# Kernel optimization log

Hardware: AMD Instinct MI355X
Metric: run time of the kernel (lower is better)

## Reference

```python
import jax, jax.numpy as jnp
import numpy as np

S, B, H = 50, 2048, 128
D = 2 * H  # bidirectional hidden width


def _xavier(k, shape):
    fan = float(sum(shape))
    return jax.random.normal(k, shape, dtype=jnp.float32) * jnp.float32(np.sqrt(2.0 / fan))


def setup_inputs() -> dict:
    key = jax.random.key(0)
    ks = jax.random.split(key, 16)
    z = lambda n: jnp.zeros((n,), jnp.float32)
    return {
        "encoder_output": jax.random.normal(ks[0], (S, B, D), jnp.float32),
        "h0": jax.random.normal(ks[1], (2, B, H), jnp.float32),
        "c0": jax.random.normal(ks[2], (2, B, H), jnp.float32),
        "restricted_k": jax.random.uniform(ks[3], (B,), jnp.float32, 0.5, 1.5),
        "W_first": _xavier(ks[4], (D, 2)), "b_first": z(D),
        "Wih_f": _xavier(ks[5], (4 * H, D)), "Whh_f": _xavier(ks[6], (4 * H, H)),
        "bih_f": z(4 * H), "bhh_f": z(4 * H),
        "Wih_b": _xavier(ks[7], (4 * H, D)), "Whh_b": _xavier(ks[8], (4 * H, H)),
        "bih_b": z(4 * H), "bhh_b": z(4 * H),
        "Wref_g": _xavier(ks[9], (D, D)), "Wq_g": _xavier(ks[10], (D, D)),
        "vg": jax.random.uniform(ks[11], (D,), jnp.float32),
        "Wref": _xavier(ks[12], (D, D)), "Wq": _xavier(ks[13], (D, D)),
        "v": jax.random.uniform(ks[14], (D,), jnp.float32),
    }


def _lstm_cell(x, h, c, Wih, Whh, bih, bhh):
    # PyTorch gate order: i, f, g, o
    g = x @ Wih.T + h @ Whh.T + bih + bhh
    i, f, gg, o = jnp.split(g, 4, axis=-1)
    c2 = jax.nn.sigmoid(f) * c + jax.nn.sigmoid(i) * jnp.tanh(gg)
    h2 = jax.nn.sigmoid(o) * jnp.tanh(c2)
    return h2, c2


def reference(encoder_output, h0, c0, restricted_k, W_first, b_first,
              Wih_f, Whh_f, bih_f, bhh_f, Wih_b, Whh_b, bih_b, bhh_b,
              Wref_g, Wq_g, vg, Wref, Wq, v):
    S_, B_, D_ = encoder_output.shape
    total_iter = S_ - 1  # mode == 'k'

    # first_entry: [1.1, 1/restricted_k] -> Linear(2, 2H) -> tanh, detached
    fe = jnp.stack([jnp.full((B_,), 1.1, jnp.float32), 1.0 / restricted_k], axis=1)
    dec_ipt0 = jax.lax.stop_gradient(jnp.tanh(fe @ W_first.T + b_first))  # [B, D]

    # ref-side attention projections are constant across decode steps
    ref_g_dot = jnp.einsum('de,sbe->bds', Wref_g, encoder_output)  # [B, D, S]
    ref_p_dot = jnp.einsum('de,sbe->bds', Wref, encoder_output)    # [B, D, S]

    mask0 = jnp.zeros((B_, S_), jnp.float32)
    NEG = -jnp.inf

    def step(carry, _):
        dec_ipt, h, c, mask = carry
        hf, cf = _lstm_cell(dec_ipt, h[0], c[0], Wih_f, Whh_f, bih_f, bhh_f)
        hb, cb = _lstm_cell(dec_ipt, h[1], c[1], Wih_b, Whh_b, bih_b, bhh_b)
        q = jnp.concatenate([hf, hb], axis=-1)  # [B, D] (len-1 bi-LSTM output)
        h2 = jnp.stack([hf, hb]); c2 = jnp.stack([cf, cb])
        maskb = mask > 0
        # glimpse attention
        u_g = jnp.einsum('d,bds->bs', vg, jnp.tanh(ref_g_dot + (q @ Wq_g.T)[:, :, None]))
        a = jax.nn.softmax(jnp.where(maskb, NEG, u_g), axis=1)  # [B, S]
        g_l = jnp.einsum('sbd,bs->bd', encoder_output, a)
        # pointer attention
        u_p = jnp.einsum('d,bds->bs', v, jnp.tanh(ref_p_dot + (g_l @ Wq.T)[:, :, None]))
        logits = jnp.where(maskb, NEG, u_p)
        sel = jnp.argmax(logits, axis=1)  # config.selection == 'argmax'
        lp = jnp.take_along_axis(jax.nn.log_softmax(logits, axis=1), sel[:, None], axis=1)[:, 0]
        mask2 = mask + jax.nn.one_hot(sel, S_, dtype=mask.dtype)
        new_ipt = encoder_output[sel, jnp.arange(B_)]  # [B, D]
        return (new_ipt, h2, c2, mask2), (sel, lp)

    _, (sels, lps) = jax.lax.scan(step, (dec_ipt0, h0, c0, mask0), None, length=total_iter)
    selections = jnp.transpose(sels)          # [B, total_iter]
    log_probs = jnp.sum(lps, axis=0)          # [B]
    return selections, log_probs
```

## Files before the change

kernel.cpp:

```cpp
#include <hip/hip_runtime.h>
#include <math.h>

#define SS 50
#define BB 2048
#define HH 128
#define DD 256
#define STEPS 49
#define NREF ((size_t)BB * SS * DD)

__device__ __forceinline__ float sigmoidf_(float x) { return 1.0f / (1.0f + expf(-x)); }

__global__ __launch_bounds__(256) void k_init(
    const float* __restrict__ h0, const float* __restrict__ c0,
    const float* __restrict__ rk, const float* __restrict__ Wf,
    const float* __restrict__ bf,
    float* __restrict__ x, float* __restrict__ q, float* __restrict__ c,
    int* __restrict__ unm, float* __restrict__ lp)
{
    int idx = blockIdx.x * 256 + threadIdx.x;
    int b = idx >> 8, d = idx & 255;
    float inv = 1.0f / rk[b];
    float t0 = 1.1f * Wf[2 * d] + inv * Wf[2 * d + 1];
    x[idx] = tanhf(t0 + bf[d]);
    q[idx] = (d < HH) ? h0[b * HH + d] : h0[BB * HH + b * HH + (d - HH)];
    c[idx] = c0[idx];
    if (idx < BB * 64) unm[idx] = idx & 63;
    if (idx < BB) lp[idx] = 0.0f;
}

__global__ __launch_bounds__(256) void k_refdot(
    const float* __restrict__ enc, const float* __restrict__ Wg,
    const float* __restrict__ Wp, const float* __restrict__ Wqq,
    float* __restrict__ refg, float* __restrict__ refp, float* __restrict__ refq)
{
    const float* W = (blockIdx.z == 0) ? Wg : (blockIdx.z == 1) ? Wp : Wqq;
    float* out = (blockIdx.z == 0) ? refg : (blockIdx.z == 1) ? refp : refq;
    __shared__ float As[16][68];
    __shared__ float Ws[16][264];
    int t = threadIdx.x;
    int m0 = blockIdx.x * 64;
    int rr = t >> 2, kk = (t & 3) << 2;
    int n = m0 + rr;
    int ab = n / SS, as = n - ab * SS;
    const float* arow = enc + ((size_t)as * BB + ab) * DD + kk;
    const float* wrow = W + (size_t)t * DD;
    int tm = (t & 15) << 2;
    int tn = (t >> 4) << 4;
    float acc[4][16];
#pragma unroll
    for (int i = 0; i < 4; i++)
#pragma unroll
        for (int j = 0; j < 16; j++) acc[i][j] = 0.0f;

    for (int k0 = 0; k0 < DD; k0 += 16) {
        float4 av = *(const float4*)(arow + k0);
        float4 w0 = *(const float4*)(wrow + k0);
        float4 w1 = *(const float4*)(wrow + k0 + 4);
        float4 w2 = *(const float4*)(wrow + k0 + 8);
        float4 w3 = *(const float4*)(wrow + k0 + 12);
        __syncthreads();
        As[kk + 0][rr] = av.x; As[kk + 1][rr] = av.y;
        As[kk + 2][rr] = av.z; As[kk + 3][rr] = av.w;
        Ws[0][t] = w0.x;  Ws[1][t] = w0.y;  Ws[2][t] = w0.z;  Ws[3][t] = w0.w;
        Ws[4][t] = w1.x;  Ws[5][t] = w1.y;  Ws[6][t] = w1.z;  Ws[7][t] = w1.w;
        Ws[8][t] = w2.x;  Ws[9][t] = w2.y;  Ws[10][t] = w2.z; Ws[11][t] = w2.w;
        Ws[12][t] = w3.x; Ws[13][t] = w3.y; Ws[14][t] = w3.z; Ws[15][t] = w3.w;
        __syncthreads();
#pragma unroll
        for (int k = 0; k < 16; k++) {
            float4 a = *(const float4*)&As[k][tm];
            float aa[4] = {a.x, a.y, a.z, a.w};
#pragma unroll
            for (int jj = 0; jj < 4; jj++) {
                float4 w = *(const float4*)&Ws[k][tn + (jj << 2)];
                float ww[4] = {w.x, w.y, w.z, w.w};
#pragma unroll
                for (int i = 0; i < 4; i++)
#pragma unroll
                    for (int cj = 0; cj < 4; cj++)
                        acc[i][jj * 4 + cj] = fmaf(aa[i], ww[cj], acc[i][jj * 4 + cj]);
            }
        }
    }
#pragma unroll
    for (int i = 0; i < 4; i++) {
        float* orow = out + (size_t)(m0 + tm + i) * DD + tn;
#pragma unroll
        for (int jj = 0; jj < 4; jj++) {
            float4 o = make_float4(acc[i][jj * 4], acc[i][jj * 4 + 1],
                                   acc[i][jj * 4 + 2], acc[i][jj * 4 + 3]);
            *(float4*)(orow + (jj << 2)) = o;
        }
    }
}

__global__ __launch_bounds__(256) void k_gates(
    const float* __restrict__ x, const float* __restrict__ q,
    const float* __restrict__ Wih_f, const float* __restrict__ Whh_f,
    const float* __restrict__ bih_f, const float* __restrict__ bhh_f,
    const float* __restrict__ Wih_b, const float* __restrict__ Whh_b,
    const float* __restrict__ bih_b, const float* __restrict__ bhh_b,
    float* __restrict__ gates)
{
    int z = blockIdx.z;
    const float* Wih = z ? Wih_b : Wih_f;
    const float* Whh = z ? Whh_b : Whh_f;
    const float* bih = z ? bih_b : bih_f;
    const float* bhh = z ? bhh_b : bhh_f;
    __shared__ float As[16][68];
    __shared__ float Ws[16][68];
    int t = threadIdx.x;
    int m0 = blockIdx.x * 64, n0 = blockIdx.y * 64;
    int rr = t >> 2, kk = (t & 3) << 2;
    int tm = (t & 15) << 2, tn = (t >> 4) << 2;
    float acc[4][4] = {};
    for (int k0 = 0; k0 < 384; k0 += 16) {
        float4 av, wv;
        if (k0 < 256) {
            av = *(const float4*)(x + (size_t)(m0 + rr) * DD + k0 + kk);
            wv = *(const float4*)(Wih + (size_t)(n0 + rr) * DD + k0 + kk);
        } else {
            av = *(const float4*)(q + (size_t)(m0 + rr) * DD + (z << 7) + (k0 - 256) + kk);
            wv = *(const float4*)(Whh + (size_t)(n0 + rr) * HH + (k0 - 256) + kk);
        }
        __syncthreads();
        As[kk + 0][rr] = av.x; As[kk + 1][rr] = av.y;
        As[kk + 2][rr] = av.z; As[kk + 3][rr] = av.w;
        Ws[kk + 0][rr] = wv.x; Ws[kk + 1][rr] = wv.y;
        Ws[kk + 2][rr] = wv.z; Ws[kk + 3][rr] = wv.w;
        __syncthreads();
#pragma unroll
        for (int k = 0; k < 16; k++) {
            float4 a = *(const float4*)&As[k][tm];
            float4 w = *(const float4*)&Ws[k][tn];
            float aa[4] = {a.x, a.y, a.z, a.w};
            float ww[4] = {w.x, w.y, w.z, w.w};
#pragma unroll
            for (int i = 0; i < 4; i++)
#pragma unroll
                for (int j = 0; j < 4; j++)
                    acc[i][j] = fmaf(aa[i], ww[j], acc[i][j]);
        }
    }
#pragma unroll
    for (int i = 0; i < 4; i++) {
        int col = n0 + tn;
        float4 o;
        o.x = acc[i][0] + bih[col + 0] + bhh[col + 0];
        o.y = acc[i][1] + bih[col + 1] + bhh[col + 1];
        o.z = acc[i][2] + bih[col + 2] + bhh[col + 2];
        o.w = acc[i][3] + bih[col + 3] + bhh[col + 3];
        *(float4*)(gates + (size_t)(m0 + tm + i) * 1024 + (z << 9) + col) = o;
    }
}

__global__ __launch_bounds__(256) void k_lstm_pw(
    const float* __restrict__ gates, float* __restrict__ q, float* __restrict__ c)
{
    int idx = blockIdx.x * 256 + threadIdx.x;
    int z = idx >> 18;
    int r = idx & (BB * HH - 1);
    int b = r >> 7, hh = r & 127;
    const float* gb = gates + (size_t)b * 1024 + (z << 9);
    float ig = sigmoidf_(gb[hh]);
    float fg = sigmoidf_(gb[128 + hh]);
    float gg = tanhf(gb[256 + hh]);
    float og = sigmoidf_(gb[384 + hh]);
    float c2 = fg * c[idx] + ig * gg;
    c[idx] = c2;
    q[(size_t)b * DD + (z << 7) + hh] = og * tanhf(c2);
}

__global__ __launch_bounds__(256) void k_proj(
    const float* __restrict__ A, const float* __restrict__ W, float* __restrict__ out)
{
    __shared__ float As[16][68];
    __shared__ float Ws[16][68];
    int t = threadIdx.x;
    int m0 = blockIdx.x * 64, n0 = blockIdx.y * 64;
    int rr = t >> 2, kk = (t & 3) << 2;
    int tm = (t & 15) << 2, tn = (t >> 4) << 2;
    const float* arow = A + (size_t)(m0 + rr) * DD + kk;
    const float* wrow = W + (size_t)(n0 + rr) * DD + kk;
    float acc[4][4] = {};
    for (int k0 = 0; k0 < DD; k0 += 16) {
        float4 av = *(const float4*)(arow + k0);
        float4 wv = *(const float4*)(wrow + k0);
        __syncthreads();
        As[kk + 0][rr] = av.x; As[kk + 1][rr] = av.y;
        As[kk + 2][rr] = av.z; As[kk + 3][rr] = av.w;
        Ws[kk + 0][rr] = wv.x; Ws[kk + 1][rr] = wv.y;
        Ws[kk + 2][rr] = wv.z; Ws[kk + 3][rr] = wv.w;
        __syncthreads();
#pragma unroll
        for (int k = 0; k < 16; k++) {
            float4 a = *(const float4*)&As[k][tm];
            float4 w = *(const float4*)&Ws[k][tn];
            float aa[4] = {a.x, a.y, a.z, a.w};
            float ww[4] = {w.x, w.y, w.z, w.w};
#pragma unroll
            for (int i = 0; i < 4; i++)
#pragma unroll
                for (int j = 0; j < 4; j++)
                    acc[i][j] = fmaf(aa[i], ww[j], acc[i][j]);
        }
    }
#pragma unroll
    for (int i = 0; i < 4; i++) {
        float4 o = make_float4(acc[i][0], acc[i][1], acc[i][2], acc[i][3]);
        *(float4*)(out + (size_t)(m0 + tm + i) * DD + n0 + tn) = o;
    }
}

__global__ __launch_bounds__(256) void k_glimpse(
    const float* __restrict__ refg, const float* __restrict__ qW,
    const float* __restrict__ vg, const float* __restrict__ enc,
    const int* __restrict__ unm, float* __restrict__ a,
    float* __restrict__ gl, int cnt)
{
    int b = blockIdx.x;
    int t = threadIdx.x, wave = t >> 6, lane = t & 63;
    __shared__ float ash[SS];
    __shared__ int sl[SS];
    if (t < cnt) sl[t] = unm[b * 64 + t];
    __syncthreads();
    int d0 = lane << 2;
    float4 qw = *(const float4*)(qW + (size_t)b * DD + d0);
    float4 vv = *(const float4*)(vg + d0);
    for (int li = wave; li < cnt; li += 4) {
        int s = sl[li];
        float4 r = *(const float4*)(refg + ((size_t)b * SS + s) * DD + d0);
        float sum = vv.x * tanhf(r.x + qw.x) + vv.y * tanhf(r.y + qw.y) +
                    vv.z * tanhf(r.z + qw.z) + vv.w * tanhf(r.w + qw.w);
#pragma unroll
        for (int off = 32; off; off >>= 1) sum += __shfl_xor(sum, off);
        if (lane == 0) ash[li] = sum;
    }
    __syncthreads();
    if (t < 64) {
        float logit = (t < cnt) ? ash[t] : -__builtin_inff();
        float m = logit;
#pragma unroll
        for (int off = 32; off; off >>= 1) m = fmaxf(m, __shfl_xor(m, off));
        float e = expf(logit - m);
        float ssum = e;
#pragma unroll
        for (int off = 32; off; off >>= 1) ssum += __shfl_xor(ssum, off);
        if (t < cnt) {
            float av = e / ssum;
            ash[t] = av;
            a[b * 64 + t] = av;
        }
    }
    __syncthreads();
    if (gl) {
        float accv = 0.0f;
        for (int li = 0; li < cnt; ++li)
            accv = fmaf(ash[li], enc[((size_t)sl[li] * BB + b) * DD + t], accv);
        gl[(size_t)b * DD + t] = accv;
    }
}

__global__ __launch_bounds__(256) void k_pointer(
    const float* __restrict__ refp, const float* __restrict__ refq,
    const float* __restrict__ gWin, const float* __restrict__ vp,
    const float* __restrict__ enc, int* __restrict__ unm,
    const float* __restrict__ a, float* __restrict__ lp,
    float* __restrict__ x, float* __restrict__ outp, int step, int cnt)
{
    int b = blockIdx.x;
    int t = threadIdx.x, wave = t >> 6, lane = t & 63;
    __shared__ float ash[SS];
    __shared__ int sl[SS];
    __shared__ float gw[DD];
    __shared__ int ssel;
    if (t < cnt) { sl[t] = unm[b * 64 + t]; ash[t] = a[b * 64 + t]; }
    __syncthreads();
    if (refq) {
        float accg = 0.0f;
        for (int li = 0; li < cnt; ++li)
            accg = fmaf(ash[li], refq[((size_t)b * SS + sl[li]) * DD + t], accg);
        gw[t] = accg;
    } else {
        gw[t] = gWin[(size_t)b * DD + t];
    }
    __syncthreads();
    int d0 = lane << 2;
    float4 g4 = *(const float4*)(gw + d0);
    float4 vv = *(const float4*)(vp + d0);
    for (int li = wave; li < cnt; li += 4) {
        int s = sl[li];
        float4 r = *(const float4*)(refp + ((size_t)b * SS + s) * DD + d0);
        float sum = vv.x * tanhf(r.x + g4.x) + vv.y * tanhf(r.y + g4.y) +
                    vv.z * tanhf(r.z + g4.z) + vv.w * tanhf(r.w + g4.w);
#pragma unroll
        for (int off = 32; off; off >>= 1) sum += __shfl_xor(sum, off);
        if (lane == 0) ash[li] = sum;
    }
    __syncthreads();
    if (t < 64) {
        float logit = (t < cnt) ? ash[t] : -__builtin_inff();
        int skey = (t < cnt) ? (sl[t] * 64 + t) : (1 << 30);
        float m = logit;
#pragma unroll
        for (int off = 32; off; off >>= 1) m = fmaxf(m, __shfl_xor(m, off));
        int cand = (logit == m) ? skey : (1 << 30);
#pragma unroll
        for (int off = 32; off; off >>= 1) cand = min(cand, __shfl_xor(cand, off));
        float e = expf(logit - m);
        float se = e;
#pragma unroll
        for (int off = 32; off; off >>= 1) se += __shfl_xor(se, off);
        if (t == 0) {
            int s_sel = cand >> 6, posl = cand & 63;
            float lpn = lp[b] - logf(se);
            lp[b] = lpn;
            outp[(size_t)b * STEPS + step] = (float)s_sel;
            if (step == STEPS - 1) outp[(size_t)BB * STEPS + b] = lpn;
            unm[b * 64 + posl] = sl[cnt - 1];
            ssel = s_sel;
        }
    }
    __syncthreads();
    x[(size_t)b * DD + t] = enc[((size_t)ssel * BB + b) * DD + t];
}

extern "C" void kernel_launch(void* const* d_in, const int* in_sizes, int n_in,
                              void* d_out, int out_size, void* d_ws, size_t ws_size,
                              hipStream_t stream) {
    const float* enc    = (const float*)d_in[0];
    const float* h0     = (const float*)d_in[1];
    const float* c0     = (const float*)d_in[2];
    const float* rk     = (const float*)d_in[3];
    const float* Wfirst = (const float*)d_in[4];
    const float* bfirst = (const float*)d_in[5];
    const float* Wih_f  = (const float*)d_in[6];
    const float* Whh_f  = (const float*)d_in[7];
    const float* bih_f  = (const float*)d_in[8];
    const float* bhh_f  = (const float*)d_in[9];
    const float* Wih_b  = (const float*)d_in[10];
    const float* Whh_b  = (const float*)d_in[11];
    const float* bih_b  = (const float*)d_in[12];
    const float* bhh_b  = (const float*)d_in[13];
    const float* Wref_g = (const float*)d_in[14];
    const float* Wq_g   = (const float*)d_in[15];
    const float* vg     = (const float*)d_in[16];
    const float* Wref   = (const float*)d_in[17];
    const float* Wq     = (const float*)d_in[18];
    const float* v      = (const float*)d_in[19];
    float* out = (float*)d_out;

    float* ws    = (float*)d_ws;
    float* refg  = ws;
    float* refp  = refg + NREF;
    float* x     = refp + NREF;
    float* q     = x + (size_t)BB * DD;
    float* c     = q + (size_t)BB * DD;
    float* gates = c + (size_t)BB * DD;
    float* qWb   = gates + (size_t)BB * 1024;
    float* gl    = qWb + (size_t)BB * DD;
    float* gWb   = gl + (size_t)BB * DD;
    float* a     = gWb + (size_t)BB * DD;
    float* lp    = a + (size_t)BB * 64;
    int*   unm   = (int*)(lp + BB);
    float* refq  = (float*)(unm + (size_t)BB * 64);

    size_t need_refq = ((size_t)(refq - ws) + NREF) * sizeof(float);
    bool useRefq = ws_size >= need_refq;

    k_init<<<dim3(BB * DD / 256), dim3(256), 0, stream>>>(h0, c0, rk, Wfirst,
                                                          bfirst, x, q, c, unm, lp);
    k_refdot<<<dim3(BB * SS / 64, 1, useRefq ? 3 : 2), dim3(256), 0, stream>>>(
        enc, Wref_g, Wref, Wq, refg, refp, refq);
    for (int step = 0; step < STEPS; ++step) {
        int cnt = SS - step;
        k_gates<<<dim3(32, 8, 2), dim3(256), 0, stream>>>(
            x, q, Wih_f, Whh_f, bih_f, bhh_f, Wih_b, Whh_b, bih_b, bhh_b, gates);
        k_lstm_pw<<<dim3(2 * BB * HH / 256), dim3(256), 0, stream>>>(gates, q, c);
        k_proj<<<dim3(32, 4), dim3(256), 0, stream>>>(q, Wq_g, qWb);
        k_glimpse<<<dim3(BB), dim3(256), 0, stream>>>(refg, qWb, vg, enc, unm, a,
                                                      useRefq ? nullptr : gl, cnt);
        if (!useRefq)
            k_proj<<<dim3(32, 4), dim3(256), 0, stream>>>(gl, Wq, gWb);
        k_pointer<<<dim3(BB), dim3(256), 0, stream>>>(refp, useRefq ? refq : nullptr,
                                                      gWb, v, enc, unm, a, lp, x, out,
                                                      step, cnt);
    }
}
```

Measured before the change: 4.834 ms.

## Fuse LSTM gate GEMM with pointwise cell and merge attention kernels

The gate GEMM now computes all four gates for a tile of hidden units so the LSTM cell update runs in its epilogue, with q double-buffered so the pointwise kernel and the gates buffer go away. The query projection, glimpse attention, pointer projection and pointer attention are merged into one per-batch-row kernel that computes q·Wq_g with a per-row matrix-vector product instead of a separate tiled GEMM. This cuts six launches per step to two and drops several intermediate global round trips. In exchange, each of the 2048 blocks rereads the full 256x256 Wq_g from cache, and the gate GEMM grid shrinks to 256 blocks.

```diff
diff --git a/kernel.cpp b/kernel.cpp
--- a/kernel.cpp
+++ b/kernel.cpp
@@ -94,151 +94,147 @@
     }
 }
 
-__global__ __launch_bounds__(256) void k_gates(
-    const float* __restrict__ x, const float* __restrict__ q,
+__global__ __launch_bounds__(256) void k_gates2(
+    const float* __restrict__ x, const float* __restrict__ qin,
     const float* __restrict__ Wih_f, const float* __restrict__ Whh_f,
     const float* __restrict__ bih_f, const float* __restrict__ bhh_f,
     const float* __restrict__ Wih_b, const float* __restrict__ Whh_b,
     const float* __restrict__ bih_b, const float* __restrict__ bhh_b,
-    float* __restrict__ gates)
+    float* __restrict__ qout, float* __restrict__ c)
 {
     int z = blockIdx.z;
     const float* Wih = z ? Wih_b : Wih_f;
     const float* Whh = z ? Whh_b : Whh_f;
     const float* bih = z ? bih_b : bih_f;
     const float* bhh = z ? bhh_b : bhh_f;
-    __shared__ float As[16][68];
-    __shared__ float Ws[16][68];
+    int m0 = blockIdx.x * 32;
+    int hc0 = blockIdx.y * 64;
     int t = threadIdx.x;
-    int m0 = blockIdx.x * 64, n0 = blockIdx.y * 64;
-    int rr = t >> 2, kk = (t & 3) << 2;
-    int tm = (t & 15) << 2, tn = (t >> 4) << 2;
-    float acc[4][4] = {};
+    int mb4 = (t >> 5) << 2;
+    int hp2 = (t & 31) << 1;
+    __shared__ float As[16][33];
+    __shared__ float Ws[16][258];
+    float acc[4][4][2] = {};
+
     for (int k0 = 0; k0 < 384; k0 += 16) {
-        float4 av, wv;
+        float4 av;
+        int am = t >> 2, ak = (t & 3) << 2;
+        if (t < 128) {
+            if (k0 < 256)
+                av = *(const float4*)(x + (size_t)(m0 + am) * DD + k0 + ak);
+            else
+                av = *(const float4*)(qin + (size_t)(m0 + am) * DD + (z << 7) + (k0 - 256) + ak);
+        }
+        int g = t >> 6, hc = t & 63;
+        int r = g * 128 + hc0 + hc;
+        float4 w0, w1, w2, w3;
         if (k0 < 256) {
-            av = *(const float4*)(x + (size_t)(m0 + rr) * DD + k0 + kk);
-            wv = *(const float4*)(Wih + (size_t)(n0 + rr) * DD + k0 + kk);
+            const float* wr = Wih + (size_t)r * DD + k0;
+            w0 = *(const float4*)(wr);     w1 = *(const float4*)(wr + 4);
+            w2 = *(const float4*)(wr + 8); w3 = *(const float4*)(wr + 12);
         } else {
-            av = *(const float4*)(q + (size_t)(m0 + rr) * DD + (z << 7) + (k0 - 256) + kk);
-            wv = *(const float4*)(Whh + (size_t)(n0 + rr) * HH + (k0 - 256) + kk);
-        }
-        __syncthreads();
-        As[kk + 0][rr] = av.x; As[kk + 1][rr] = av.y;
-        As[kk + 2][rr] = av.z; As[kk + 3][rr] = av.w;
-        Ws[kk + 0][rr] = wv.x; Ws[kk + 1][rr] = wv.y;
-        Ws[kk + 2][rr] = wv.z; Ws[kk + 3][rr] = wv.w;
-        __syncthreads();
-#pragma unroll
-        for (int k = 0; k < 16; k++) {
-            float4 a = *(const float4*)&As[k][tm];
-            float4 w = *(const float4*)&Ws[k][tn];
-            float aa[4] = {a.x, a.y, a.z, a.w};
-            float ww[4] = {w.x, w.y, w.z, w.w};
-#pragma unroll
-            for (int i = 0; i < 4; i++)
-#pragma unroll
-                for (int j = 0; j < 4; j++)
-                    acc[i][j] = fmaf(aa[i], ww[j], acc[i][j]);
-        }
-    }
-#pragma unroll
-    for (int i = 0; i < 4; i++) {
-        int col = n0 + tn;
-        float4 o;
-        o.x = acc[i][0] + bih[col + 0] + bhh[col + 0];
-        o.y = acc[i][1] + bih[col + 1] + bhh[col + 1];
-        o.z = acc[i][2] + bih[col + 2] + bhh[col + 2];
-        o.w = acc[i][3] + bih[col + 3] + bhh[col + 3];
-        *(float4*)(gates + (size_t)(m0 + tm + i) * 1024 + (z << 9) + col) = o;
-    }
-}
-
-__global__ __launch_bounds__(256) void k_lstm_pw(
-    const float* __restrict__ gates, float* __restrict__ q, float* __restrict__ c)
+            const float* wr = Whh + (size_t)r * HH + (k0 - 256);
+            w0 = *(const float4*)(wr);     w1 = *(const float4*)(wr + 4);
+            w2 = *(const float4*)(wr + 8); w3 = *(const float4*)(wr + 12);
+        }
+        __syncthreads();
+        if (t < 128) {
+            As[ak + 0][am] = av.x; As[ak + 1][am] = av.y;
+            As[ak + 2][am] = av.z; As[ak + 3][am] = av.w;
+        }
+        Ws[0][t] = w0.x;  Ws[1][t] = w0.y;  Ws[2][t] = w0.z;  Ws[3][t] = w0.w;
+        Ws[4][t] = w1.x;  Ws[5][t] = w1.y;  Ws[6][t] = w1.z;  Ws[7][t] = w1.w;
+        Ws[8][t] = w2.x;  Ws[9][t] = w2.y;  Ws[10][t] = w2.z; Ws[11][t] = w2.w;
+        Ws[12][t] = w3.x; Ws[13][t] = w3.y; Ws[14][t] = w3.z; Ws[15][t] = w3.w;
+        __syncthreads();
+#pragma unroll
+        for (int k = 0; k < 16; ++k) {
+            float a0 = As[k][mb4 + 0];
+            float a1 = As[k][mb4 + 1];
+            float a2 = As[k][mb4 + 2];
+            float a3 = As[k][mb4 + 3];
+#pragma unroll
+            for (int g2 = 0; g2 < 4; ++g2) {
+                float2 wv = *(const float2*)&Ws[k][(g2 << 6) + hp2];
+                acc[0][g2][0] = fmaf(a0, wv.x, acc[0][g2][0]);
+                acc[0][g2][1] = fmaf(a0, wv.y, acc[0][g2][1]);
+                acc[1][g2][0] = fmaf(a1, wv.x, acc[1][g2][0]);
+                acc[1][g2][1] = fmaf(a1, wv.y, acc[1][g2][1]);
+                acc[2][g2][0] = fmaf(a2, wv.x, acc[2][g2][0]);
+                acc[2][g2][1] = fmaf(a2, wv.y, acc[2][g2][1]);
+                acc[3][g2][0] = fmaf(a3, wv.x, acc[3][g2][0]);
+                acc[3][g2][1] = fmaf(a3, wv.y, acc[3][g2][1]);
+            }
+        }
+    }
+#pragma unroll
+    for (int i = 0; i < 4; ++i) {
+#pragma unroll
+        for (int cc = 0; cc < 2; ++cc) {
+            int b = m0 + mb4 + i;
+            int h = hc0 + hp2 + cc;
+            float gi = acc[i][0][cc] + bih[h]       + bhh[h];
+            float gf = acc[i][1][cc] + bih[128 + h] + bhh[128 + h];
+            float gg = acc[i][2][cc] + bih[256 + h] + bhh[256 + h];
+            float go = acc[i][3][cc] + bih[384 + h] + bhh[384 + h];
+            size_t cidx = (size_t)z * BB * HH + (size_t)b * HH + h;
+            float c2 = sigmoidf_(gf) * c[cidx] + sigmoidf_(gi) * tanhf(gg);
+            c[cidx] = c2;
+            qout[(size_t)b * DD + (z << 7) + h] = sigmoidf_(go) * tanhf(c2);
+        }
+    }
+}
+
+__global__ __launch_bounds__(256) void k_attn(
+    const float* __restrict__ refg, const float* __restrict__ refp,
+    const float* __restrict__ refq, const float* __restrict__ q,
+    const float* __restrict__ Wqg, const float* __restrict__ vg,
+    const float* __restrict__ Wqp, const float* __restrict__ vp,
+    const float* __restrict__ enc, int* __restrict__ unm,
+    float* __restrict__ lp, float* __restrict__ x,
+    float* __restrict__ outp, int step, int cnt)
 {
-    int idx = blockIdx.x * 256 + threadIdx.x;
-    int z = idx >> 18;
-    int r = idx & (BB * HH - 1);
-    int b = r >> 7, hh = r & 127;
-    const float* gb = gates + (size_t)b * 1024 + (z << 9);
-    float ig = sigmoidf_(gb[hh]);
-    float fg = sigmoidf_(gb[128 + hh]);
-    float gg = tanhf(gb[256 + hh]);
-    float og = sigmoidf_(gb[384 + hh]);
-    float c2 = fg * c[idx] + ig * gg;
-    c[idx] = c2;
-    q[(size_t)b * DD + (z << 7) + hh] = og * tanhf(c2);
-}
-
-__global__ __launch_bounds__(256) void k_proj(
-    const float* __restrict__ A, const float* __restrict__ W, float* __restrict__ out)
-{
-    __shared__ float As[16][68];
-    __shared__ float Ws[16][68];
-    int t = threadIdx.x;
-    int m0 = blockIdx.x * 64, n0 = blockIdx.y * 64;
-    int rr = t >> 2, kk = (t & 3) << 2;
-    int tm = (t & 15) << 2, tn = (t >> 4) << 2;
-    const float* arow = A + (size_t)(m0 + rr) * DD + kk;
-    const float* wrow = W + (size_t)(n0 + rr) * DD + kk;
-    float acc[4][4] = {};
-    for (int k0 = 0; k0 < DD; k0 += 16) {
-        float4 av = *(const float4*)(arow + k0);
-        float4 wv = *(const float4*)(wrow + k0);
-        __syncthreads();
-        As[kk + 0][rr] = av.x; As[kk + 1][rr] = av.y;
-        As[kk + 2][rr] = av.z; As[kk + 3][rr] = av.w;
-        Ws[kk + 0][rr] = wv.x; Ws[kk + 1][rr] = wv.y;
-        Ws[kk + 2][rr] = wv.z; Ws[kk + 3][rr] = wv.w;
-        __syncthreads();
-#pragma unroll
-        for (int k = 0; k < 16; k++) {
-            float4 a = *(const float4*)&As[k][tm];
-            float4 w = *(const float4*)&Ws[k][tn];
-            float aa[4] = {a.x, a.y, a.z, a.w};
-            float ww[4] = {w.x, w.y, w.z, w.w};
-#pragma unroll
-            for (int i = 0; i < 4; i++)
-#pragma unroll
-                for (int j = 0; j < 4; j++)
-                    acc[i][j] = fmaf(aa[i], ww[j], acc[i][j]);
-        }
-    }
-#pragma unroll
-    for (int i = 0; i < 4; i++) {
-        float4 o = make_float4(acc[i][0], acc[i][1], acc[i][2], acc[i][3]);
-        *(float4*)(out + (size_t)(m0 + tm + i) * DD + n0 + tn) = o;
-    }
-}
-
-__global__ __launch_bounds__(256) void k_glimpse(
-    const float* __restrict__ refg, const float* __restrict__ qW,
-    const float* __restrict__ vg, const float* __restrict__ enc,
-    const int* __restrict__ unm, float* __restrict__ a,
-    float* __restrict__ gl, int cnt)
-{
-    int b = blockIdx.x;
-    int t = threadIdx.x, wave = t >> 6, lane = t & 63;
-    __shared__ float ash[SS];
-    __shared__ int sl[SS];
+    int b = blockIdx.x, t = threadIdx.x;
+    int wave = t >> 6, lane = t & 63;
+    __shared__ float qsh[DD];
+    __shared__ float qw[DD];
+    __shared__ float gw[DD];
+    __shared__ float uu[64];
+    __shared__ float aa[64];
+    __shared__ int sl[64];
+    __shared__ int ssel;
     if (t < cnt) sl[t] = unm[b * 64 + t];
+    qsh[t] = q[(size_t)b * DD + t];
+    __syncthreads();
+    {
+        const float* wr = Wqg + (size_t)t * DD;
+        float s0 = 0, s1 = 0, s2 = 0, s3 = 0;
+        for (int e = 0; e < DD; e += 4) {
+            float4 w = *(const float4*)(wr + e);
+            float4 qv = *(const float4*)(qsh + e);
+            s0 = fmaf(w.x, qv.x, s0); s1 = fmaf(w.y, qv.y, s1);
+            s2 = fmaf(w.z, qv.z, s2); s3 = fmaf(w.w, qv.w, s3);
+        }
+        qw[t] = (s0 + s1) + (s2 + s3);
+    }
     __syncthreads();
     int d0 = lane << 2;
-    float4 qw = *(const float4*)(qW + (size_t)b * DD + d0);
-    float4 vv = *(const float4*)(vg + d0);
-    for (int li = wave; li < cnt; li += 4) {
-        int s = sl[li];
-        float4 r = *(const float4*)(refg + ((size_t)b * SS + s) * DD + d0);
-        float sum = vv.x * tanhf(r.x + qw.x) + vv.y * tanhf(r.y + qw.y) +
-                    vv.z * tanhf(r.z + qw.z) + vv.w * tanhf(r.w + qw.w);
-#pragma unroll
-        for (int off = 32; off; off >>= 1) sum += __shfl_xor(sum, off);
-        if (lane == 0) ash[li] = sum;
+    {
+        float4 vvg = *(const float4*)(vg + d0);
+        float4 qw4 = *(const float4*)(&qw[d0]);
+        for (int li = wave; li < cnt; li += 4) {
+            int s = sl[li];
+            float4 r = *(const float4*)(refg + ((size_t)b * SS + s) * DD + d0);
+            float sum = vvg.x * tanhf(r.x + qw4.x) + vvg.y * tanhf(r.y + qw4.y) +
+                        vvg.z * tanhf(r.z + qw4.z) + vvg.w * tanhf(r.w + qw4.w);
+#pragma unroll
+            for (int off = 32; off; off >>= 1) sum += __shfl_xor(sum, off);
+            if (lane == 0) uu[li] = sum;
+        }
     }
     __syncthreads();
     if (t < 64) {
-        float logit = (t < cnt) ? ash[t] : -__builtin_inff();
+        float logit = (t < cnt) ? uu[t] : -__builtin_inff();
         float m = logit;
 #pragma unroll
         for (int off = 32; off; off >>= 1) m = fmaxf(m, __shfl_xor(m, off));
@@ -246,60 +242,47 @@
         float ssum = e;
 #pragma unroll
         for (int off = 32; off; off >>= 1) ssum += __shfl_xor(ssum, off);
-        if (t < cnt) {
-            float av = e / ssum;
-            ash[t] = av;
-            a[b * 64 + t] = av;
-        }
-    }
-    __syncthreads();
-    if (gl) {
-        float accv = 0.0f;
-        for (int li = 0; li < cnt; ++li)
-            accv = fmaf(ash[li], enc[((size_t)sl[li] * BB + b) * DD + t], accv);
-        gl[(size_t)b * DD + t] = accv;
-    }
-}
-
-__global__ __launch_bounds__(256) void k_pointer(
-    const float* __restrict__ refp, const float* __restrict__ refq,
-    const float* __restrict__ gWin, const float* __restrict__ vp,
-    const float* __restrict__ enc, int* __restrict__ unm,
-    const float* __restrict__ a, float* __restrict__ lp,
-    float* __restrict__ x, float* __restrict__ outp, int step, int cnt)
-{
-    int b = blockIdx.x;
-    int t = threadIdx.x, wave = t >> 6, lane = t & 63;
-    __shared__ float ash[SS];
-    __shared__ int sl[SS];
-    __shared__ float gw[DD];
-    __shared__ int ssel;
-    if (t < cnt) { sl[t] = unm[b * 64 + t]; ash[t] = a[b * 64 + t]; }
+        if (t < cnt) aa[t] = e / ssum;
+    }
     __syncthreads();
     if (refq) {
         float accg = 0.0f;
         for (int li = 0; li < cnt; ++li)
-            accg = fmaf(ash[li], refq[((size_t)b * SS + sl[li]) * DD + t], accg);
+            accg = fmaf(aa[li], refq[((size_t)b * SS + sl[li]) * DD + t], accg);
         gw[t] = accg;
     } else {
-        gw[t] = gWin[(size_t)b * DD + t];
-    }
-    __syncthreads();
-    int d0 = lane << 2;
-    float4 g4 = *(const float4*)(gw + d0);
-    float4 vv = *(const float4*)(vp + d0);
-    for (int li = wave; li < cnt; li += 4) {
-        int s = sl[li];
-        float4 r = *(const float4*)(refp + ((size_t)b * SS + s) * DD + d0);
-        float sum = vv.x * tanhf(r.x + g4.x) + vv.y * tanhf(r.y + g4.y) +
-                    vv.z * tanhf(r.z + g4.z) + vv.w * tanhf(r.w + g4.w);
-#pragma unroll
-        for (int off = 32; off; off >>= 1) sum += __shfl_xor(sum, off);
-        if (lane == 0) ash[li] = sum;
+        float accl = 0.0f;
+        for (int li = 0; li < cnt; ++li)
+            accl = fmaf(aa[li], enc[((size_t)sl[li] * BB + b) * DD + t], accl);
+        qsh[t] = accl;
+        __syncthreads();
+        const float* wr = Wqp + (size_t)t * DD;
+        float s0 = 0, s1 = 0, s2 = 0, s3 = 0;
+        for (int e = 0; e < DD; e += 4) {
+            float4 w = *(const float4*)(wr + e);
+            float4 gv = *(const float4*)(qsh + e);
+            s0 = fmaf(w.x, gv.x, s0); s1 = fmaf(w.y, gv.y, s1);
+            s2 = fmaf(w.z, gv.z, s2); s3 = fmaf(w.w, gv.w, s3);
+        }
+        gw[t] = (s0 + s1) + (s2 + s3);
+    }
+    __syncthreads();
+    {
+        float4 vvp = *(const float4*)(vp + d0);
+        float4 gw4 = *(const float4*)(&gw[d0]);
+        for (int li = wave; li < cnt; li += 4) {
+            int s = sl[li];
+            float4 r = *(const float4*)(refp + ((size_t)b * SS + s) * DD + d0);
+            float sum = vvp.x * tanhf(r.x + gw4.x) + vvp.y * tanhf(r.y + gw4.y) +
+                        vvp.z * tanhf(r.z + gw4.z) + vvp.w * tanhf(r.w + gw4.w);
+#pragma unroll
+            for (int off = 32; off; off >>= 1) sum += __shfl_xor(sum, off);
+            if (lane == 0) uu[li] = sum;
+        }
     }
     __syncthreads();
     if (t < 64) {
-        float logit = (t < cnt) ? ash[t] : -__builtin_inff();
+        float logit = (t < cnt) ? uu[t] : -__builtin_inff();
         int skey = (t < cnt) ? (sl[t] * 64 + t) : (1 << 30);
         float m = logit;
 #pragma unroll
@@ -350,40 +333,33 @@
     const float* v      = (const float*)d_in[19];
     float* out = (float*)d_out;
 
-    float* ws    = (float*)d_ws;
-    float* refg  = ws;
-    float* refp  = refg + NREF;
-    float* x     = refp + NREF;
-    float* q     = x + (size_t)BB * DD;
-    float* c     = q + (size_t)BB * DD;
-    float* gates = c + (size_t)BB * DD;
-    float* qWb   = gates + (size_t)BB * 1024;
-    float* gl    = qWb + (size_t)BB * DD;
-    float* gWb   = gl + (size_t)BB * DD;
-    float* a     = gWb + (size_t)BB * DD;
-    float* lp    = a + (size_t)BB * 64;
-    int*   unm   = (int*)(lp + BB);
-    float* refq  = (float*)(unm + (size_t)BB * 64);
+    float* ws   = (float*)d_ws;
+    float* refg = ws;
+    float* refp = refg + NREF;
+    float* x    = refp + NREF;
+    float* qA   = x + (size_t)BB * DD;
+    float* qB   = qA + (size_t)BB * DD;
+    float* c    = qB + (size_t)BB * DD;
+    float* lp   = c + (size_t)2 * BB * HH;
+    int*   unm  = (int*)(lp + BB);
+    float* refq = (float*)(unm + (size_t)BB * 64);
 
     size_t need_refq = ((size_t)(refq - ws) + NREF) * sizeof(float);
     bool useRefq = ws_size >= need_refq;
+    const float* refq_arg = useRefq ? refq : nullptr;
 
     k_init<<<dim3(BB * DD / 256), dim3(256), 0, stream>>>(h0, c0, rk, Wfirst,
-                                                          bfirst, x, q, c, unm, lp);
+                                                          bfirst, x, qA, c, unm, lp);
     k_refdot<<<dim3(BB * SS / 64, 1, useRefq ? 3 : 2), dim3(256), 0, stream>>>(
         enc, Wref_g, Wref, Wq, refg, refp, refq);
     for (int step = 0; step < STEPS; ++step) {
         int cnt = SS - step;
-        k_gates<<<dim3(32, 8, 2), dim3(256), 0, stream>>>(
-            x, q, Wih_f, Whh_f, bih_f, bhh_f, Wih_b, Whh_b, bih_b, bhh_b, gates);
-        k_lstm_pw<<<dim3(2 * BB * HH / 256), dim3(256), 0, stream>>>(gates, q, c);
-        k_proj<<<dim3(32, 4), dim3(256), 0, stream>>>(q, Wq_g, qWb);
-        k_glimpse<<<dim3(BB), dim3(256), 0, stream>>>(refg, qWb, vg, enc, unm, a,
-                                                      useRefq ? nullptr : gl, cnt);
-        if (!useRefq)
-            k_proj<<<dim3(32, 4), dim3(256), 0, stream>>>(gl, Wq, gWb);
-        k_pointer<<<dim3(BB), dim3(256), 0, stream>>>(refp, useRefq ? refq : nullptr,
-                                                      gWb, v, enc, unm, a, lp, x, out,
-                                                      step, cnt);
-    }
-}
+        float* qin  = (step & 1) ? qB : qA;
+        float* qout = (step & 1) ? qA : qB;
+        k_gates2<<<dim3(64, 2, 2), dim3(256), 0, stream>>>(
+            x, qin, Wih_f, Whh_f, bih_f, bhh_f, Wih_b, Whh_b, bih_b, bhh_b, qout, c);
+        k_attn<<<dim3(BB), dim3(256), 0, stream>>>(
+            refg, refp, refq_arg, qout, Wq_g, vg, Wq, v, enc, unm, lp, x, out,
+            step, cnt);
+    }
+}
```

Measured after the change: 9.143 ms. 1.89x slower.

## Fuse glimpse and pointer attention into one kernel; enlarge refdot row tile

Applied to the files above, without the earlier changes.

When the precomputed enc·Wq projection (refq) fits in the workspace, the per-step glimpse and pointer kernels become a single k_attn2 kernel per batch row. It computes glimpse scores, softmax, the glimpse projection as an attention-weighted sum of refq rows, pointer scores, argmax, log-prob and the next-input gather without round-tripping intermediates through global memory. This removes one kernel launch per step and the write and reload of the glimpse weights between kernels. Separately, the refdot GEMM now gives each thread 8 rows instead of 4 (128-row tiles), which raises register use and may lower occupancy. The gates buffer offset is also rewritten as 2*BB*HH, which equals the previous BB*DD.

```diff
diff --git a/kernel.cpp b/kernel.cpp
--- a/kernel.cpp
+++ b/kernel.cpp
@@ -35,32 +35,37 @@
 {
     const float* W = (blockIdx.z == 0) ? Wg : (blockIdx.z == 1) ? Wp : Wqq;
     float* out = (blockIdx.z == 0) ? refg : (blockIdx.z == 1) ? refp : refq;
-    __shared__ float As[16][68];
+    __shared__ float As[16][132];
     __shared__ float Ws[16][264];
     int t = threadIdx.x;
-    int m0 = blockIdx.x * 64;
+    int m0 = blockIdx.x * 128;
     int rr = t >> 2, kk = (t & 3) << 2;
-    int n = m0 + rr;
-    int ab = n / SS, as = n - ab * SS;
-    const float* arow = enc + ((size_t)as * BB + ab) * DD + kk;
+    int n0 = m0 + rr, n1 = m0 + 64 + rr;
+    int ab0 = n0 / SS, as0 = n0 - ab0 * SS;
+    int ab1 = n1 / SS, as1 = n1 - ab1 * SS;
+    const float* arow0 = enc + ((size_t)as0 * BB + ab0) * DD + kk;
+    const float* arow1 = enc + ((size_t)as1 * BB + ab1) * DD + kk;
     const float* wrow = W + (size_t)t * DD;
     int tm = (t & 15) << 2;
     int tn = (t >> 4) << 4;
-    float acc[4][16];
-#pragma unroll
-    for (int i = 0; i < 4; i++)
+    float acc[8][16];
+#pragma unroll
+    for (int i = 0; i < 8; i++)
 #pragma unroll
         for (int j = 0; j < 16; j++) acc[i][j] = 0.0f;
 
     for (int k0 = 0; k0 < DD; k0 += 16) {
-        float4 av = *(const float4*)(arow + k0);
+        float4 a0 = *(const float4*)(arow0 + k0);
+        float4 a1 = *(const float4*)(arow1 + k0);
         float4 w0 = *(const float4*)(wrow + k0);
         float4 w1 = *(const float4*)(wrow + k0 + 4);
         float4 w2 = *(const float4*)(wrow + k0 + 8);
         float4 w3 = *(const float4*)(wrow + k0 + 12);
         __syncthreads();
-        As[kk + 0][rr] = av.x; As[kk + 1][rr] = av.y;
-        As[kk + 2][rr] = av.z; As[kk + 3][rr] = av.w;
+        As[kk + 0][rr] = a0.x; As[kk + 1][rr] = a0.y;
+        As[kk + 2][rr] = a0.z; As[kk + 3][rr] = a0.w;
+        As[kk + 0][64 + rr] = a1.x; As[kk + 1][64 + rr] = a1.y;
+        As[kk + 2][64 + rr] = a1.z; As[kk + 3][64 + rr] = a1.w;
         Ws[0][t] = w0.x;  Ws[1][t] = w0.y;  Ws[2][t] = w0.z;  Ws[3][t] = w0.w;
         Ws[4][t] = w1.x;  Ws[5][t] = w1.y;  Ws[6][t] = w1.z;  Ws[7][t] = w1.w;
         Ws[8][t] = w2.x;  Ws[9][t] = w2.y;  Ws[10][t] = w2.z; Ws[11][t] = w2.w;
@@ -68,14 +73,15 @@
         __syncthreads();
 #pragma unroll
         for (int k = 0; k < 16; k++) {
-            float4 a = *(const float4*)&As[k][tm];
-            float aa[4] = {a.x, a.y, a.z, a.w};
+            float4 alo = *(const float4*)&As[k][tm];
+            float4 ahi = *(const float4*)&As[k][64 + tm];
+            float aa[8] = {alo.x, alo.y, alo.z, alo.w, ahi.x, ahi.y, ahi.z, ahi.w};
 #pragma unroll
             for (int jj = 0; jj < 4; jj++) {
                 float4 w = *(const float4*)&Ws[k][tn + (jj << 2)];
                 float ww[4] = {w.x, w.y, w.z, w.w};
 #pragma unroll
-                for (int i = 0; i < 4; i++)
+                for (int i = 0; i < 8; i++)
 #pragma unroll
                     for (int cj = 0; cj < 4; cj++)
                         acc[i][jj * 4 + cj] = fmaf(aa[i], ww[cj], acc[i][jj * 4 + cj]);
@@ -83,8 +89,9 @@
         }
     }
 #pragma unroll
-    for (int i = 0; i < 4; i++) {
-        float* orow = out + (size_t)(m0 + tm + i) * DD + tn;
+    for (int i = 0; i < 8; i++) {
+        int row = (i < 4) ? (m0 + tm + i) : (m0 + 64 + tm + (i - 4));
+        float* orow = out + (size_t)row * DD + tn;
 #pragma unroll
         for (int jj = 0; jj < 4; jj++) {
             float4 o = make_float4(acc[i][jj * 4], acc[i][jj * 4 + 1],
@@ -210,6 +217,98 @@
         float4 o = make_float4(acc[i][0], acc[i][1], acc[i][2], acc[i][3]);
         *(float4*)(out + (size_t)(m0 + tm + i) * DD + n0 + tn) = o;
     }
+}
+
+__global__ __launch_bounds__(256) void k_attn2(
+    const float* __restrict__ refg, const float* __restrict__ refp,
+    const float* __restrict__ refq, const float* __restrict__ qW,
+    const float* __restrict__ vg, const float* __restrict__ vp,
+    const float* __restrict__ enc, int* __restrict__ unm,
+    float* __restrict__ lp, float* __restrict__ x,
+    float* __restrict__ outp, int step, int cnt)
+{
+    int b = blockIdx.x, t = threadIdx.x;
+    int wave = t >> 6, lane = t & 63;
+    __shared__ float uu[64];
+    __shared__ float aa[64];
+    __shared__ float gw[DD];
+    __shared__ int sl[64];
+    __shared__ int ssel;
+    if (t < cnt) sl[t] = unm[b * 64 + t];
+    __syncthreads();
+    int d0 = lane << 2;
+    {
+        float4 vvg = *(const float4*)(vg + d0);
+        float4 qw4 = *(const float4*)(qW + (size_t)b * DD + d0);
+        for (int li = wave; li < cnt; li += 4) {
+            int s = sl[li];
+            float4 r = *(const float4*)(refg + ((size_t)b * SS + s) * DD + d0);
+            float sum = vvg.x * tanhf(r.x + qw4.x) + vvg.y * tanhf(r.y + qw4.y) +
+                        vvg.z * tanhf(r.z + qw4.z) + vvg.w * tanhf(r.w + qw4.w);
+#pragma unroll
+            for (int off = 32; off; off >>= 1) sum += __shfl_xor(sum, off);
+            if (lane == 0) uu[li] = sum;
+        }
+    }
+    __syncthreads();
+    if (t < 64) {
+        float logit = (t < cnt) ? uu[t] : -__builtin_inff();
+        float m = logit;
+#pragma unroll
+        for (int off = 32; off; off >>= 1) m = fmaxf(m, __shfl_xor(m, off));
+        float e = expf(logit - m);
+        float ssum = e;
+#pragma unroll
+        for (int off = 32; off; off >>= 1) ssum += __shfl_xor(ssum, off);
+        if (t < cnt) aa[t] = e / ssum;
+    }
+    __syncthreads();
+    {
+        float accg = 0.0f;
+        for (int li = 0; li < cnt; ++li)
+            accg = fmaf(aa[li], refq[((size_t)b * SS + sl[li]) * DD + t], accg);
+        gw[t] = accg;
+    }
+    __syncthreads();
+    {
+        float4 vvp = *(const float4*)(vp + d0);
+        float4 gw4 = *(const float4*)(&gw[d0]);
+        for (int li = wave; li < cnt; li += 4) {
+            int s = sl[li];
+            float4 r = *(const float4*)(refp + ((size_t)b * SS + s) * DD + d0);
+            float sum = vvp.x * tanhf(r.x + gw4.x) + vvp.y * tanhf(r.y + gw4.y) +
+                        vvp.z * tanhf(r.z + gw4.z) + vvp.w * tanhf(r.w + gw4.w);
+#pragma unroll
+            for (int off = 32; off; off >>= 1) sum += __shfl_xor(sum, off);
+            if (lane == 0) uu[li] = sum;
+        }
+    }
+    __syncthreads();
+    if (t < 64) {
+        float logit = (t < cnt) ? uu[t] : -__builtin_inff();
+        int skey = (t < cnt) ? (sl[t] * 64 + t) : (1 << 30);
+        float m = logit;
+#pragma unroll
+        for (int off = 32; off; off >>= 1) m = fmaxf(m, __shfl_xor(m, off));
+        int cand = (logit == m) ? skey : (1 << 30);
+#pragma unroll
+        for (int off = 32; off; off >>= 1) cand = min(cand, __shfl_xor(cand, off));
+        float e = expf(logit - m);
+        float se = e;
+#pragma unroll
+        for (int off = 32; off; off >>= 1) se += __shfl_xor(se, off);
+        if (t == 0) {
+            int s_sel = cand >> 6, posl = cand & 63;
+            float lpn = lp[b] - logf(se);
+            lp[b] = lpn;
+            outp[(size_t)b * STEPS + step] = (float)s_sel;
+            if (step == STEPS - 1) outp[(size_t)BB * STEPS + b] = lpn;
+            unm[b * 64 + posl] = sl[cnt - 1];
+            ssel = s_sel;
+        }
+    }
+    __syncthreads();
+    x[(size_t)b * DD + t] = enc[((size_t)ssel * BB + b) * DD + t];
 }
 
 __global__ __launch_bounds__(256) void k_glimpse(
@@ -356,7 +455,7 @@
     float* x     = refp + NREF;
     float* q     = x + (size_t)BB * DD;
     float* c     = q + (size_t)BB * DD;
-    float* gates = c + (size_t)BB * DD;
+    float* gates = c + (size_t)2 * BB * HH;
     float* qWb   = gates + (size_t)BB * 1024;
     float* gl    = qWb + (size_t)BB * DD;
     float* gWb   = gl + (size_t)BB * DD;
@@ -370,7 +469,7 @@
 
     k_init<<<dim3(BB * DD / 256), dim3(256), 0, stream>>>(h0, c0, rk, Wfirst,
                                                           bfirst, x, q, c, unm, lp);
-    k_refdot<<<dim3(BB * SS / 64, 1, useRefq ? 3 : 2), dim3(256), 0, stream>>>(
+    k_refdot<<<dim3(BB * SS / 128, 1, useRefq ? 3 : 2), dim3(256), 0, stream>>>(
         enc, Wref_g, Wref, Wq, refg, refp, refq);
     for (int step = 0; step < STEPS; ++step) {
         int cnt = SS - step;
@@ -378,12 +477,15 @@
             x, q, Wih_f, Whh_f, bih_f, bhh_f, Wih_b, Whh_b, bih_b, bhh_b, gates);
         k_lstm_pw<<<dim3(2 * BB * HH / 256), dim3(256), 0, stream>>>(gates, q, c);
         k_proj<<<dim3(32, 4), dim3(256), 0, stream>>>(q, Wq_g, qWb);
-        k_glimpse<<<dim3(BB), dim3(256), 0, stream>>>(refg, qWb, vg, enc, unm, a,
-                                                      useRefq ? nullptr : gl, cnt);
-        if (!useRefq)
+        if (useRefq) {
+            k_attn2<<<dim3(BB), dim3(256), 0, stream>>>(
+                refg, refp, refq, qWb, vg, v, enc, unm, lp, x, out, step, cnt);
+        } else {
+            k_glimpse<<<dim3(BB), dim3(256), 0, stream>>>(refg, qWb, vg, enc, unm, a,
+                                                          gl, cnt);
             k_proj<<<dim3(32, 4), dim3(256), 0, stream>>>(gl, Wq, gWb);
-        k_pointer<<<dim3(BB), dim3(256), 0, stream>>>(refp, useRefq ? refq : nullptr,
-                                                      gWb, v, enc, unm, a, lp, x, out,
-                                                      step, cnt);
-    }
-}
+            k_pointer<<<dim3(BB), dim3(256), 0, stream>>>(refp, nullptr, gWb, v, enc,
+                                                          unm, a, lp, x, out, step, cnt);
+        }
+    }
+}
```

Result: faster. 4.650 ms (-3.8%).
